# Performance work log

Hardware: AMD Instinct MI355X
Metric: run time of the kernel (lower is better)

The kernel has to match this reference:

```python
import jax, jax.numpy as jnp
import numpy as np

EMBED_DIM = 1024
ATTEN_DIM = 64


def setup_inputs() -> dict:
    key = jax.random.key(0)
    k_x, k_q, k_k, k_v = jax.random.split(key, 4)
    B, S = 4, 4096
    scale = 1.0 / np.sqrt(EMBED_DIM)
    x = jax.random.normal(k_x, (B, S, EMBED_DIM), dtype=jnp.float32)
    # torch nn.Linear weights are [out_features, in_features]
    Wq = jax.random.normal(k_q, (ATTEN_DIM, EMBED_DIM), dtype=jnp.float32) * scale
    Wk = jax.random.normal(k_k, (ATTEN_DIM, EMBED_DIM), dtype=jnp.float32) * scale
    Wv = jax.random.normal(k_v, (ATTEN_DIM, EMBED_DIM), dtype=jnp.float32) * scale
    return {"x": x, "Wq": Wq, "Wk": Wk, "Wv": Wv}


def reference(x, Wq, Wk, Wv):
    # q, k, v: [B, S, D]
    q = jnp.einsum('bse,de->bsd', x, Wq)
    k = jnp.einsum('bse,de->bsd', x, Wk)
    v = jnp.einsum('bse,de->bsd', x, Wv)
    d = k.shape[-1]
    scores = jnp.einsum('bsd,btd->bst', q, k) / jnp.sqrt(jnp.float32(d))
    S = x.shape[1]
    causal = jnp.tril(jnp.ones((S, S), dtype=bool))
    scores = jnp.where(causal[None, :, :], scores, -jnp.inf)
    attn = jax.nn.softmax(scores, axis=-1)
    return jnp.einsum('bst,btd->bsd', attn, v)
```

## Files before the change

kernel.cpp:

```cpp
#include <hip/hip_runtime.h>
#include <hip/hip_bf16.h>
#include <stdint.h>

typedef __attribute__((ext_vector_type(8))) short  short8;
typedef __attribute__((ext_vector_type(4))) short  short4v;
typedef __attribute__((ext_vector_type(4))) float  float4v;

#define MFMA16(a, b, c) __builtin_amdgcn_mfma_f32_16x16x32_bf16((a), (b), (c), 0, 0, 0)

#define S_LEN  4096
#define NBATCH 4
#define EMB    1024
#define DD     64
#define NROWS  (NBATCH * S_LEN)
#define SCL2   0.1803368801111204f

#define AS1 const __attribute__((address_space(1))) unsigned int*
#define AS3 __attribute__((address_space(3))) unsigned int*

static __device__ __forceinline__ short f2bf(float f) {
  uint32_t u = __float_as_uint(f);
  return (short)((u + 0x7FFFu + ((u >> 16) & 1u)) >> 16);
}
static __device__ __forceinline__ unsigned pk2(float a, float b) {
  union { __hip_bfloat162 h; unsigned u; } z;
  z.h = __float22bfloat162_rn(make_float2(a, b));
  return z.u;
}
static __device__ __forceinline__ short8 cvt8(float4v a, float4v b) {
  union { unsigned u[4]; short8 s; } z;
  z.u[0] = pk2(a[0], a[1]); z.u[1] = pk2(a[2], a[3]);
  z.u[2] = pk2(b[0], b[1]); z.u[3] = pk2(b[2], b[3]);
  return z.s;
}

__global__ void wcvt_kernel(const float* __restrict__ Wq, const float* __restrict__ Wk,
                            const float* __restrict__ Wv, short* __restrict__ Wb2) {
  const int t   = blockIdx.x * 256 + threadIdx.x;
  const int row = t >> 7;
  const int k   = (t & 127) * 8;
  const float* src = (row < 64) ? (Wq + (size_t)row * EMB)
                   : (row < 128) ? (Wk + (size_t)(row - 64) * EMB)
                                 : (Wv + (size_t)(row - 128) * EMB);
  const float sc = (row < 64) ? SCL2 : 1.0f;
  float4v a = *(const float4v*)(src + k);
  float4v b = *(const float4v*)(src + k + 4);
#pragma unroll
  for (int i = 0; i < 4; ++i) { a[i] *= sc; b[i] *= sc; }
  *(short8*)(Wb2 + (((k >> 5) * 192 + row) << 5) + (k & 31)) = cvt8(a, b);
}

__global__ __launch_bounds__(256, 2) void qkv_kernel(
    const float* __restrict__ x, const short* __restrict__ Wb2,
    short* __restrict__ Qb, short* __restrict__ Kb, short* __restrict__ Vt) {
  __shared__ float As[2][2048];
  __shared__ short Bs[2][12288];

  const int tid  = threadIdx.x;
  const int w    = tid >> 6;
  const int lane = tid & 63;
  const int ln   = lane & 15;
  const int quad = lane >> 4;
  const int m0   = blockIdx.x * 32;
  const int wr   = w & 1;
  const int wc   = w >> 1;

  const int tA0 = 2 * w, tA1 = 2 * w + 1;
  const float* xA0 = x + (size_t)(m0 + ((tA0 >> 2) << 4) + (lane >> 2)) * EMB
                       + ((tA0 & 3) * 4 + (lane & 3)) * 4;
  const float* xA1 = x + (size_t)(m0 + ((tA1 >> 2) << 4) + (lane >> 2)) * EMB
                       + ((tA1 & 3) * 4 + (lane & 3)) * 4;
  const short* wB = Wb2 + (size_t)(6 * w) * 512 + lane * 8;

#define STAGE(S, BUF) do {                                                      \
    __builtin_amdgcn_global_load_lds((AS1)(xA0 + (S) * 64),                     \
        (AS3)&As[BUF][tA0 * 256], 16, 0, 0);                                    \
    __builtin_amdgcn_global_load_lds((AS1)(xA1 + (S) * 64),                     \
        (AS3)&As[BUF][tA1 * 256], 16, 0, 0);                                    \
    _Pragma("unroll")                                                           \
    for (int j = 0; j < 6; ++j)                                                 \
      __builtin_amdgcn_global_load_lds((AS1)(wB + (size_t)(S) * 12288 + j * 512),\
          (AS3)&Bs[BUF][(6 * w + j) * 512], 16, 0, 0);                          \
  } while (0)

  const float4v zz = {0.f, 0.f, 0.f, 0.f};
  float4v acc[6] = {zz, zz, zz, zz, zz, zz};

  STAGE(0, 0);
  int buf = 0;
  for (int s = 0; s < 16; ++s) {
    __syncthreads();
    if (s + 1 < 16) STAGE(s + 1, buf ^ 1);
    short8 aF[2];
#pragma unroll
    for (int h = 0; h < 2; ++h) {
      const int ai = (wr * 4 + 2 * h + (quad >> 1)) * 256 + (ln * 4 + (quad & 1) * 2) * 4;
      const float4v lo = *(const float4v*)&As[buf][ai];
      const float4v hi = *(const float4v*)&As[buf][ai + 4];
      aF[h] = cvt8(lo, hi);
    }
#pragma unroll
    for (int f = 0; f < 6; ++f) {
      const int cf = wc * 6 + f;
      const short8 b0 = *(const short8*)&Bs[buf][(cf * 16 + ln) * 32 + quad * 8];
      const short8 b1 = *(const short8*)&Bs[buf][6144 + (cf * 16 + ln) * 32 + quad * 8];
      if (wc == 0 || f < 2) {
        acc[f] = MFMA16(aF[0], b0, acc[f]);
        acc[f] = MFMA16(aF[1], b1, acc[f]);
      } else {
        acc[f] = MFMA16(b0, aF[0], acc[f]);
        acc[f] = MFMA16(b1, aF[1], acc[f]);
      }
    }
    buf ^= 1;
  }
#undef STAGE

  const int b  = m0 >> 12;
  const int sb = m0 & (S_LEN - 1);
  if (wc == 0) {
#pragma unroll
    for (int f = 0; f < 6; ++f)
#pragma unroll
      for (int r = 0; r < 4; ++r) {
        const int row = m0 + wr * 16 + quad * 4 + r;
        if (f < 4) Qb[(size_t)row * DD + f * 16 + ln] = f2bf(acc[f][r]);
        else       Kb[(size_t)row * DD + (f - 4) * 16 + ln] = f2bf(acc[f][r]);
      }
  } else {
#pragma unroll
    for (int f = 0; f < 2; ++f)
#pragma unroll
      for (int r = 0; r < 4; ++r) {
        const int row = m0 + wr * 16 + quad * 4 + r;
        Kb[(size_t)row * DD + 32 + f * 16 + ln] = f2bf(acc[f][r]);
      }
#pragma unroll
    for (int f = 2; f < 6; ++f)
#pragma unroll
      for (int r = 0; r < 4; ++r) {
        const int d = (f - 2) * 16 + quad * 4 + r;
        Vt[((size_t)b * DD + d) * S_LEN + sb + wr * 16 + ln] = f2bf(acc[f][r]);
      }
  }
}

#define PSTRW 34

__global__ __launch_bounds__(256, 1) void attn_kernel(
    const short* __restrict__ Qb, const short* __restrict__ Kb,
    const short* __restrict__ Vt, float* __restrict__ out) {
  __shared__ short kvbuf[4][3][4096];
  __shared__ float pbuf[4][32 * PSTRW];
  __shared__ float llds[4][32];

  const int tid  = threadIdx.x;
  const int w    = tid >> 6;
  const int lane = tid & 63;
  const int ln   = lane & 15;
  const int quad = lane >> 4;
  const int g    = blockIdx.x;
  const int b    = g & 3;
  const int j    = g >> 2;

  const short* Kbase = Kb + (size_t)b * S_LEN * DD;
  const short* Vbase = Vt + (size_t)b * DD * S_LEN;
  const int    klane = (lane >> 3) * DD + (((lane & 7) ^ (lane >> 3))) * 8;
  const size_t vlane = (size_t)(lane >> 2) * S_LEN + (((lane & 3) ^ ((lane >> 2) & 3))) * 8;
  float* pw = &pbuf[w][0];
  const float4v zz = {0.f, 0.f, 0.f, 0.f};

#define KVSTAGE(KV0, BUF) do {                                                  \
    const short* kp_ = Kbase + (size_t)(KV0) * DD + klane;                      \
    const short* vp_ = Vbase + (KV0) + vlane;                                   \
    _Pragma("unroll")                                                           \
    for (int s5 = 0; s5 < 4; ++s5)                                              \
      __builtin_amdgcn_global_load_lds((AS1)(kp_ + s5 * 8 * DD),                \
          (AS3)&kvbuf[w][BUF][s5 * 512], 16, 0, 0);                             \
    _Pragma("unroll")                                                           \
    for (int s5 = 0; s5 < 4; ++s5)                                              \
      __builtin_amdgcn_global_load_lds((AS1)(vp_ + (size_t)(s5 * 16) * S_LEN),  \
          (AS3)&kvbuf[w][BUF][2048 + s5 * 512], 16, 0, 0);                      \
  } while (0)

  for (int ph = 0; ph < 2; ++ph) {
    const int band = ph ? (127 - j) : j;
    const int qb   = band * 32;
    const int qg0  = b * S_LEN + qb;
    const int T    = band + 1;

    short8 aQ[2][2];
#pragma unroll
    for (int rfi = 0; rfi < 2; ++rfi)
#pragma unroll
      for (int h = 0; h < 2; ++h)
        aQ[rfi][h] = *(const short8*)(Qb + (size_t)(qg0 + rfi * 16 + ln) * DD + h * 32 + quad * 8);

    float4v o[2][4];
    float lp[2][4];
#pragma unroll
    for (int rfi = 0; rfi < 2; ++rfi)
#pragma unroll
      for (int d = 0; d < 4; ++d) { o[rfi][d] = zz; lp[rfi][d] = 0.f; }

    if (w < T)     KVSTAGE(w * 32, 0);
    if (w + 4 < T) KVSTAGE((w + 4) * 32, 1);
    int nbuf = 0;

    for (int it = w; it < T; it += 4) {
      const int kv0 = it * 32;
      if (it + 4 < T) { asm volatile("s_waitcnt vmcnt(8)" ::: "memory"); }
      else            { asm volatile("s_waitcnt vmcnt(0)" ::: "memory"); }
      const short* kb_ = &kvbuf[w][nbuf][0];
      const short* vb_ = &kvbuf[w][nbuf][2048];

      short8 kf[2][2];
#pragma unroll
      for (int ct = 0; ct < 2; ++ct)
#pragma unroll
        for (int h = 0; h < 2; ++h)
          kf[ct][h] = *(const short8*)(kb_ + (2 * ct + (ln >> 3)) * 512
                                           + (ln & 7) * 64 + (((h * 4 + quad) ^ (ln & 7))) * 8);
      short8 vf[4];
#pragma unroll
      for (int dt = 0; dt < 4; ++dt)
        vf[dt] = *(const short8*)(vb_ + dt * 512 + ln * 32 + ((quad ^ (ln & 3))) * 8);
      asm volatile("s_waitcnt lgkmcnt(0)" ::: "memory");

      if (it + 8 < T) KVSTAGE((it + 8) * 32, (nbuf + 2 >= 3) ? (nbuf - 1) : (nbuf + 2));

      float4v s[2][2];
#pragma unroll
      for (int rfi = 0; rfi < 2; ++rfi)
#pragma unroll
        for (int ct = 0; ct < 2; ++ct) {
          s[rfi][ct] = MFMA16(aQ[rfi][0], kf[ct][0], zz);
          s[rfi][ct] = MFMA16(aQ[rfi][1], kf[ct][1], s[rfi][ct]);
        }

      if (it == band) {
#pragma unroll
        for (int rfi = 0; rfi < 2; ++rfi)
#pragma unroll
          for (int ct = 0; ct < 2; ++ct)
#pragma unroll
            for (int r = 0; r < 4; ++r) {
              float e = __builtin_amdgcn_exp2f(fminf(s[rfi][ct][r], 60.0f));
              if (kv0 + ct * 16 + ln > qb + rfi * 16 + quad * 4 + r) e = 0.f;
              s[rfi][ct][r] = e;
            }
      } else {
#pragma unroll
        for (int rfi = 0; rfi < 2; ++rfi)
#pragma unroll
          for (int ct = 0; ct < 2; ++ct)
#pragma unroll
            for (int r = 0; r < 4; ++r)
              s[rfi][ct][r] = __builtin_amdgcn_exp2f(fminf(s[rfi][ct][r], 60.0f));
      }
#pragma unroll
      for (int rfi = 0; rfi < 2; ++rfi)
#pragma unroll
        for (int r = 0; r < 4; ++r)
          lp[rfi][r] += s[rfi][0][r] + s[rfi][1][r];

#pragma unroll
      for (int rfi = 0; rfi < 2; ++rfi)
#pragma unroll
        for (int ct = 0; ct < 2; ++ct)
#pragma unroll
          for (int r = 0; r < 4; ++r)
            pw[(rfi * 16 + quad * 4 + r) * PSTRW + ct * 16 + ln] = s[rfi][ct][r];
      asm volatile("s_waitcnt lgkmcnt(0)" ::: "memory");
      short8 aP[2];
#pragma unroll
      for (int rfi = 0; rfi < 2; ++rfi) {
        const float4v lo = *(const float4v*)&pw[(rfi * 16 + ln) * PSTRW + quad * 8];
        const float4v hi = *(const float4v*)&pw[(rfi * 16 + ln) * PSTRW + quad * 8 + 4];
        aP[rfi] = cvt8(lo, hi);
      }
#pragma unroll
      for (int rfi = 0; rfi < 2; ++rfi)
#pragma unroll
        for (int dt = 0; dt < 4; ++dt)
          o[rfi][dt] = MFMA16(aP[rfi], vf[dt], o[rfi][dt]);

      nbuf = (nbuf + 1 >= 3) ? 0 : nbuf + 1;
    }

#pragma unroll
    for (int rfi = 0; rfi < 2; ++rfi)
#pragma unroll
      for (int r = 0; r < 4; ++r) {
        float lr = lp[rfi][r];
        lr += __shfl_xor(lr, 1);
        lr += __shfl_xor(lr, 2);
        lr += __shfl_xor(lr, 4);
        lr += __shfl_xor(lr, 8);
        if (ln == 0) llds[w][rfi * 16 + quad * 4 + r] = lr;
      }
    float* ow = (float*)&kvbuf[w][0][0];
#pragma unroll
    for (int rfi = 0; rfi < 2; ++rfi)
#pragma unroll
      for (int dt = 0; dt < 4; ++dt)
#pragma unroll
        for (int r = 0; r < 4; ++r)
          ow[(rfi * 16 + quad * 4 + r) * 64 + dt * 16 + ln] = o[rfi][dt][r];
    __syncthreads();

#pragma unroll
    for (int jj = 0; jj < 8; ++jj) {
      const int idx = tid + jj * 256;
      const int row = idx >> 6, col = idx & 63;
      float sum = 0.f, lt = 0.f;
#pragma unroll
      for (int wi = 0; wi < 4; ++wi) {
        sum += ((const float*)&kvbuf[wi][0][0])[row * 64 + col];
        lt  += llds[wi][row];
      }
      out[(size_t)(qg0 + row) * DD + col] = sum * __builtin_amdgcn_rcpf(lt);
    }
    __syncthreads();
  }
#undef KVSTAGE
}

extern "C" void kernel_launch(void* const* d_in, const int* in_sizes, int n_in,
                              void* d_out, int out_size, void* d_ws, size_t ws_size,
                              hipStream_t stream) {
  const float* x  = (const float*)d_in[0];
  const float* Wq = (const float*)d_in[1];
  const float* Wk = (const float*)d_in[2];
  const float* Wv = (const float*)d_in[3];

  short* Qb  = (short*)d_ws;
  short* Kb  = Qb + (size_t)NROWS * DD;
  short* Vt  = Kb + (size_t)NROWS * DD;
  short* Wb2 = Vt + (size_t)NROWS * DD;

  wcvt_kernel<<<dim3(96), dim3(256), 0, stream>>>(Wq, Wk, Wv, Wb2);
  qkv_kernel<<<dim3(NROWS / 32), dim3(256), 0, stream>>>(x, Wb2, Qb, Kb, Vt);
  attn_kernel<<<dim3(NBATCH * 64), dim3(256), 0, stream>>>(Qb, Kb, Vt, (float*)d_out);
}
```

Baseline: 162.1 us.

## Split causal attention KV loop across 16 waves with direct global loads

Raises the attention block from 4 to 16 wavefronts. The causal KV tiles are strided across all 16 waves and their partial outputs and row sums are reduced through a larger LDS buffer. The triple-buffered global_load_lds prefetch of K/V tiles into LDS is removed: each wave now reads its K and V fragments straight from global memory into registers. The aim is more in-flight waves per CU to hide latency and a simpler loop, at the cost of losing explicit prefetch and making the final 16-way reduction heavier. The launch-bounds hint of four 1024-thread blocks per CU could also squeeze the register budget.

```diff
diff --git a/kernel.cpp b/kernel.cpp
--- a/kernel.cpp
+++ b/kernel.cpp
@@ -145,14 +145,11 @@
   }
 }
 
-#define PSTRW 34
-
-__global__ __launch_bounds__(256, 1) void attn_kernel(
+__global__ __launch_bounds__(1024, 4) void attn_kernel(
     const short* __restrict__ Qb, const short* __restrict__ Kb,
     const short* __restrict__ Vt, float* __restrict__ out) {
-  __shared__ short kvbuf[4][3][4096];
-  __shared__ float pbuf[4][32 * PSTRW];
-  __shared__ float llds[4][32];
+  __shared__ float Obuf[16][2048];
+  __shared__ float llds[16][32];
 
   const int tid  = threadIdx.x;
   const int w    = tid >> 6;
@@ -165,23 +162,8 @@
 
   const short* Kbase = Kb + (size_t)b * S_LEN * DD;
   const short* Vbase = Vt + (size_t)b * DD * S_LEN;
-  const int    klane = (lane >> 3) * DD + (((lane & 7) ^ (lane >> 3))) * 8;
-  const size_t vlane = (size_t)(lane >> 2) * S_LEN + (((lane & 3) ^ ((lane >> 2) & 3))) * 8;
-  float* pw = &pbuf[w][0];
+  float* pw = &Obuf[w][0];
   const float4v zz = {0.f, 0.f, 0.f, 0.f};
-
-#define KVSTAGE(KV0, BUF) do {                                                  \
-    const short* kp_ = Kbase + (size_t)(KV0) * DD + klane;                      \
-    const short* vp_ = Vbase + (KV0) + vlane;                                   \
-    _Pragma("unroll")                                                           \
-    for (int s5 = 0; s5 < 4; ++s5)                                              \
-      __builtin_amdgcn_global_load_lds((AS1)(kp_ + s5 * 8 * DD),                \
-          (AS3)&kvbuf[w][BUF][s5 * 512], 16, 0, 0);                             \
-    _Pragma("unroll")                                                           \
-    for (int s5 = 0; s5 < 4; ++s5)                                              \
-      __builtin_amdgcn_global_load_lds((AS1)(vp_ + (size_t)(s5 * 16) * S_LEN),  \
-          (AS3)&kvbuf[w][BUF][2048 + s5 * 512], 16, 0, 0);                      \
-  } while (0)
 
   for (int ph = 0; ph < 2; ++ph) {
     const int band = ph ? (127 - j) : j;
@@ -203,31 +185,18 @@
 #pragma unroll
       for (int d = 0; d < 4; ++d) { o[rfi][d] = zz; lp[rfi][d] = 0.f; }
 
-    if (w < T)     KVSTAGE(w * 32, 0);
-    if (w + 4 < T) KVSTAGE((w + 4) * 32, 1);
-    int nbuf = 0;
-
-    for (int it = w; it < T; it += 4) {
+    for (int it = w; it < T; it += 16) {
       const int kv0 = it * 32;
-      if (it + 4 < T) { asm volatile("s_waitcnt vmcnt(8)" ::: "memory"); }
-      else            { asm volatile("s_waitcnt vmcnt(0)" ::: "memory"); }
-      const short* kb_ = &kvbuf[w][nbuf][0];
-      const short* vb_ = &kvbuf[w][nbuf][2048];
-
       short8 kf[2][2];
 #pragma unroll
       for (int ct = 0; ct < 2; ++ct)
 #pragma unroll
         for (int h = 0; h < 2; ++h)
-          kf[ct][h] = *(const short8*)(kb_ + (2 * ct + (ln >> 3)) * 512
-                                           + (ln & 7) * 64 + (((h * 4 + quad) ^ (ln & 7))) * 8);
+          kf[ct][h] = *(const short8*)(Kbase + (size_t)(kv0 + ct * 16 + ln) * DD + h * 32 + quad * 8);
       short8 vf[4];
 #pragma unroll
       for (int dt = 0; dt < 4; ++dt)
-        vf[dt] = *(const short8*)(vb_ + dt * 512 + ln * 32 + ((quad ^ (ln & 3))) * 8);
-      asm volatile("s_waitcnt lgkmcnt(0)" ::: "memory");
-
-      if (it + 8 < T) KVSTAGE((it + 8) * 32, (nbuf + 2 >= 3) ? (nbuf - 1) : (nbuf + 2));
+        vf[dt] = *(const short8*)(Vbase + (size_t)(dt * 16 + ln) * S_LEN + kv0 + quad * 8);
 
       float4v s[2][2];
 #pragma unroll
@@ -270,13 +239,13 @@
         for (int ct = 0; ct < 2; ++ct)
 #pragma unroll
           for (int r = 0; r < 4; ++r)
-            pw[(rfi * 16 + quad * 4 + r) * PSTRW + ct * 16 + ln] = s[rfi][ct][r];
+            pw[(rfi * 16 + quad * 4 + r) * 36 + ct * 16 + ln] = s[rfi][ct][r];
       asm volatile("s_waitcnt lgkmcnt(0)" ::: "memory");
       short8 aP[2];
 #pragma unroll
       for (int rfi = 0; rfi < 2; ++rfi) {
-        const float4v lo = *(const float4v*)&pw[(rfi * 16 + ln) * PSTRW + quad * 8];
-        const float4v hi = *(const float4v*)&pw[(rfi * 16 + ln) * PSTRW + quad * 8 + 4];
+        const float4v lo = *(const float4v*)&pw[(rfi * 16 + ln) * 36 + quad * 8];
+        const float4v hi = *(const float4v*)&pw[(rfi * 16 + ln) * 36 + quad * 8 + 4];
         aP[rfi] = cvt8(lo, hi);
       }
 #pragma unroll
@@ -284,8 +253,6 @@
 #pragma unroll
         for (int dt = 0; dt < 4; ++dt)
           o[rfi][dt] = MFMA16(aP[rfi], vf[dt], o[rfi][dt]);
-
-      nbuf = (nbuf + 1 >= 3) ? 0 : nbuf + 1;
     }
 
 #pragma unroll
@@ -298,32 +265,26 @@
         lr += __shfl_xor(lr, 4);
         lr += __shfl_xor(lr, 8);
         if (ln == 0) llds[w][rfi * 16 + quad * 4 + r] = lr;
-      }
-    float* ow = (float*)&kvbuf[w][0][0];
-#pragma unroll
-    for (int rfi = 0; rfi < 2; ++rfi)
-#pragma unroll
-      for (int dt = 0; dt < 4; ++dt)
-#pragma unroll
-        for (int r = 0; r < 4; ++r)
-          ow[(rfi * 16 + quad * 4 + r) * 64 + dt * 16 + ln] = o[rfi][dt][r];
+#pragma unroll
+        for (int dt = 0; dt < 4; ++dt)
+          Obuf[w][(rfi * 16 + quad * 4 + r) * 64 + dt * 16 + ln] = o[rfi][dt][r];
+      }
     __syncthreads();
 
 #pragma unroll
-    for (int jj = 0; jj < 8; ++jj) {
-      const int idx = tid + jj * 256;
+    for (int jj = 0; jj < 2; ++jj) {
+      const int idx = tid + jj * 1024;
       const int row = idx >> 6, col = idx & 63;
       float sum = 0.f, lt = 0.f;
 #pragma unroll
-      for (int wi = 0; wi < 4; ++wi) {
-        sum += ((const float*)&kvbuf[wi][0][0])[row * 64 + col];
+      for (int wi = 0; wi < 16; ++wi) {
+        sum += Obuf[wi][idx];
         lt  += llds[wi][row];
       }
       out[(size_t)(qg0 + row) * DD + col] = sum * __builtin_amdgcn_rcpf(lt);
     }
     __syncthreads();
   }
-#undef KVSTAGE
 }
 
 extern "C" void kernel_launch(void* const* d_in, const int* in_sizes, int n_in,
@@ -341,5 +302,5 @@
 
   wcvt_kernel<<<dim3(96), dim3(256), 0, stream>>>(Wq, Wk, Wv, Wb2);
   qkv_kernel<<<dim3(NROWS / 32), dim3(256), 0, stream>>>(x, Wb2, Qb, Kb, Vt);
-  attn_kernel<<<dim3(NBATCH * 64), dim3(256), 0, stream>>>(Qb, Kb, Vt, (float*)d_out);
-}
+  attn_kernel<<<dim3(NBATCH * 64), dim3(1024), 0, stream>>>(Qb, Kb, Vt, (float*)d_out);
+}
```

Result: no change. 164.6 us (+1.6%).
